# Performance work log

Hardware: AMD Instinct MI355X
Metric: run time of the kernel (lower is better)

## Reference

```python
import jax, jax.numpy as jnp
import numpy as np

N = 8192
K = 8192
BS = 128  # quantization block size (elements per codebook)
NE = 8    # codebook entries per block (3-bit indices)


def setup_inputs() -> dict:
    key = jax.random.key(0)
    k1, k2, k3 = jax.random.split(key, 3)
    num_blocks = N * K // BS  # 524288
    n_packed_bytes = num_blocks * BS * 3 // 8  # 25165824
    x = jax.random.normal(k1, (2048, K), dtype=jnp.float32)
    # random packed bytes (values 0..255) -> uniformly random 3-bit indices
    packed_indices = jax.random.randint(k2, (n_packed_bytes,), 0, 256, dtype=jnp.int32)
    codebook = jax.random.normal(k3, (num_blocks, NE), dtype=jnp.float32)
    return {"x": x, "packed_indices": packed_indices, "codebook": codebook}


def _dequantize(packed_indices, codebook):
    num_blocks = codebook.shape[0]
    packed = packed_indices.reshape(-1, 3).astype(jnp.int32)  # (n_groups, 3)
    bits24 = packed[:, 0] | (packed[:, 1] << 8) | (packed[:, 2] << 16)
    shifts = jnp.arange(8, dtype=jnp.int32) * 3
    idx = (bits24[:, None] >> shifts[None, :]) & 7          # (n_groups, 8)
    idx = idx.reshape(num_blocks, BS)                        # (num_blocks, BS)
    # per-block codebook gather: w[b, i] = codebook[b, idx[b, i]]
    w = jnp.take_along_axis(codebook, idx, axis=1)           # (num_blocks, BS)
    return w.reshape(N, K)


def reference(x, packed_indices, codebook):
    w = _dequantize(packed_indices, codebook)  # (N, K) fp32
    y = x @ w.T                                # (batch, N)
    return y
```

## Files before the change

### kernel.cpp

```cpp
#include <hip/hip_runtime.h>
#include <hip/hip_bf16.h>

#define Mdim 2048
#define Ndim 8192
#define Kdim 8192
#define NT (Kdim / 64)

typedef __bf16 bf16x8 __attribute__((ext_vector_type(8)));
typedef float f32x4 __attribute__((ext_vector_type(4)));
typedef unsigned short ushort8 __attribute__((ext_vector_type(8)));
typedef unsigned short ushort4v __attribute__((ext_vector_type(4)));

__device__ __forceinline__ unsigned short f2bf_rne(float f) {
    unsigned u = __float_as_uint(f);
    u += 0x7fffu + ((u >> 16) & 1u);
    return (unsigned short)(u >> 16);
}

__device__ __forceinline__ ushort8 decode8(unsigned bits, float4 c0, float4 c1) {
    ushort8 o;
#pragma unroll
    for (int i = 0; i < 8; ++i) {
        unsigned id = (bits >> (3 * i)) & 7u;
        float a0 = (id & 1) ? c0.y : c0.x;
        float a1 = (id & 1) ? c0.w : c0.z;
        float a2 = (id & 1) ? c1.y : c1.x;
        float a3 = (id & 1) ? c1.w : c1.z;
        float b0 = (id & 2) ? a1 : a0;
        float b1 = (id & 2) ? a3 : a2;
        float v  = (id & 4) ? b1 : b0;
        o[i] = f2bf_rne(v);
    }
    return o;
}

__global__ __launch_bounds__(256) void k_prep(const int* __restrict__ packed,
                                              const float* __restrict__ cb,
                                              const float* __restrict__ x,
                                              unsigned short* __restrict__ W,
                                              unsigned short* __restrict__ xb) {
    const int t = threadIdx.x;
    if (blockIdx.x < 16384) {
        const size_t th = (size_t)blockIdx.x * 256 + t;
        const size_t g0 = th * 2;
        const int2* pv = (const int2*)(packed + g0 * 3);
        int2 q0 = pv[0], q1 = pv[1], q2 = pv[2];
        unsigned bits0 = (unsigned)(q0.x & 255) | ((unsigned)(q0.y & 255) << 8) |
                         ((unsigned)(q1.x & 255) << 16);
        unsigned bits1 = (unsigned)(q1.y & 255) | ((unsigned)(q2.x & 255) << 8) |
                         ((unsigned)(q2.y & 255) << 16);
        const float4* cv0 = (const float4*)(cb + ((g0 >> 4) << 3));
        const float4* cv1 = (const float4*)(cb + (((g0 + 1) >> 4) << 3));
        float4 c00 = cv0[0], c01 = cv0[1];
        float4 c10 = cv1[0], c11 = cv1[1];
        ushort8 o0 = decode8(bits0, c00, c01);
        ushort8 o1 = decode8(bits1, c10, c11);
        unsigned short* wp = W + (g0 << 3);
        *(ushort8*)(wp)     = o0;
        *(ushort8*)(wp + 8) = o1;
    } else {
        const size_t u = (size_t)(blockIdx.x - 16384) * 256 + t;
        float4 a = ((const float4*)x)[u];
        ushort4v o;
        o[0] = f2bf_rne(a.x); o[1] = f2bf_rne(a.y);
        o[2] = f2bf_rne(a.z); o[3] = f2bf_rne(a.w);
        ((ushort4v*)xb)[u] = o;
    }
}

__device__ __forceinline__ void gld16(const unsigned short* g, unsigned short* l) {
    __builtin_amdgcn_global_load_lds(
        (const __attribute__((address_space(1))) unsigned int*)g,
        (__attribute__((address_space(3))) unsigned int*)l, 16, 0, 0);
}

#define BAR()    asm volatile("s_barrier" ::: "memory")
#define FENCE()  asm volatile("" ::: "memory")
#define WAIT_DS0() asm volatile("s_waitcnt lgkmcnt(0)" ::: "memory")

__global__ __launch_bounds__(512, 2) void k_gemm(const unsigned short* __restrict__ A,
                                                 const unsigned short* __restrict__ B,
                                                 float* __restrict__ C) {
    __shared__ unsigned short LA[4 * 8192];
    __shared__ unsigned short LB[4 * 8192];

    const int tid  = threadIdx.x;
    const int lane = tid & 63;
    const int wave = tid >> 6;
    const int qm = wave >> 2;
    const int qn = wave & 3;

    const int bid = blockIdx.x;
    const int bm = (bid & 7) * 256;
    const int bn = (bid >> 3) * 256;

    const int chunk0 = tid, chunk1 = tid + 512;
    const int srow0 = chunk0 >> 3, srow1 = chunk1 >> 3;
    const int scol0 = ((chunk0 & 7) ^ (srow0 & 7)) * 8;
    const int scol1 = ((chunk1 & 7) ^ (srow1 & 7)) * 8;
    const unsigned short* Ag0 = A + (size_t)(bm + srow0) * Kdim + scol0;
    const unsigned short* Ag1 = A + (size_t)(bm + srow1) * Kdim + scol1;
    const unsigned short* Bg0 = B + (size_t)(bn + srow0) * Kdim + scol0;
    const unsigned short* Bg1 = B + (size_t)(bn + srow1) * Kdim + scol1;

#define STAGE_A(T, H, BUF) do {                                                   \
    unsigned short* _d = LA + ((BUF) * 2 + (H)) * 8192;                           \
    gld16(Ag0 + (size_t)(H) * 128 * Kdim + (size_t)(T) * 64, _d + (size_t)tid * 8);        \
    gld16(Ag1 + (size_t)(H) * 128 * Kdim + (size_t)(T) * 64, _d + (size_t)(tid + 512) * 8);\
    FENCE();                                                                      \
} while (0)
#define STAGE_B(T, H, BUF) do {                                                   \
    unsigned short* _d = LB + ((BUF) * 2 + (H)) * 8192;                           \
    gld16(Bg0 + (size_t)(H) * 128 * Kdim + (size_t)(T) * 64, _d + (size_t)tid * 8);        \
    gld16(Bg1 + (size_t)(H) * 128 * Kdim + (size_t)(T) * 64, _d + (size_t)(tid + 512) * 8);\
    FENCE();                                                                      \
} while (0)

    const int r15 = lane & 15;
    const int q   = lane >> 4;
    const int rlo = r15 & 7;
    const int aro = qm * 64 + r15;
    const int bro = qn * 32 + r15;
    const int ch0 = ((0 + q) ^ rlo) * 8;
    const int ch1 = ((4 + q) ^ rlo) * 8;

    f32x4 acc[4][4][2];
    const f32x4 zero = {0.f, 0.f, 0.f, 0.f};
#pragma unroll
    for (int p = 0; p < 4; ++p)
#pragma unroll
        for (int i = 0; i < 4; ++i)
#pragma unroll
            for (int j = 0; j < 2; ++j) acc[p][i][j] = zero;

    bf16x8 af[4][2], bf[2][2];

#define LOAD_A(BUF, H) do {                                                       \
    const unsigned short* _s = LA + ((BUF) * 2 + (H)) * 8192;                     \
    _Pragma("unroll") for (int i = 0; i < 4; ++i) {                               \
        int _r = (aro + i * 16) * 64;                                             \
        af[i][0] = *(const bf16x8*)&_s[_r + ch0];                                 \
        af[i][1] = *(const bf16x8*)&_s[_r + ch1];                                 \
    }                                                                             \
} while (0)
#define LOAD_B(BUF, H) do {                                                       \
    const unsigned short* _s = LB + ((BUF) * 2 + (H)) * 8192;                     \
    _Pragma("unroll") for (int j = 0; j < 2; ++j) {                               \
        int _r = (bro + j * 16) * 64;                                             \
        bf[j][0] = *(const bf16x8*)&_s[_r + ch0];                                 \
        bf[j][1] = *(const bf16x8*)&_s[_r + ch1];                                 \
    }                                                                             \
} while (0)

#define MFMA_PHASE(P) do {                                                        \
    __builtin_amdgcn_s_setprio(1);                                                \
    _Pragma("unroll") for (int i = 0; i < 4; ++i)                                 \
    _Pragma("unroll") for (int j = 0; j < 2; ++j) {                               \
        acc[P][i][j] = __builtin_amdgcn_mfma_f32_16x16x32_bf16(                   \
            af[i][0], bf[j][0], acc[P][i][j], 0, 0, 0);                           \
        acc[P][i][j] = __builtin_amdgcn_mfma_f32_16x16x32_bf16(                   \
            af[i][1], bf[j][1], acc[P][i][j], 0, 0, 0);                           \
    }                                                                             \
    __builtin_amdgcn_s_setprio(0);                                                \
} while (0)

#define KSTEP(T, BUF) do {                                                        \
    LOAD_A(BUF, 0); LOAD_B(BUF, 0);                                               \
    if ((T) + 1 < NT) STAGE_B((T) + 1, 0, (BUF) ^ 1);                             \
    BAR(); WAIT_DS0();                                                            \
    MFMA_PHASE(0);                                                                \
    BAR();                                                                        \
    LOAD_B(BUF, 1);                                                               \
    if ((T) + 2 < NT) STAGE_A((T) + 2, 0, BUF);                                   \
    BAR(); WAIT_DS0();                                                            \
    MFMA_PHASE(1);                                                                \
    BAR();                                                                        \
    LOAD_A(BUF, 1);                                                               \
    if ((T) + 2 < NT) STAGE_B((T) + 2, 1, BUF);                                   \
    BAR(); WAIT_DS0();                                                            \
    MFMA_PHASE(2);                                                                \
    BAR();                                                                        \
    LOAD_B(BUF, 0);                                                               \
    if ((T) + 2 < NT) STAGE_A((T) + 2, 1, BUF);                                   \
    BAR(); WAIT_DS0();                                                            \
    MFMA_PHASE(3);                                                                \
    if ((T) + 2 < NT) { asm volatile("s_waitcnt vmcnt(6)" ::: "memory"); }        \
    else              { asm volatile("s_waitcnt vmcnt(0)" ::: "memory"); }        \
    BAR();                                                                        \
} while (0)

    STAGE_A(0, 0, 0); STAGE_B(0, 1, 0); STAGE_A(0, 1, 0); STAGE_B(0, 0, 0);
    STAGE_A(1, 0, 1); STAGE_B(1, 1, 1); STAGE_A(1, 1, 1);
    asm volatile("s_waitcnt vmcnt(6)" ::: "memory");
    BAR();

    for (int t2 = 0; t2 < NT; t2 += 2) {
        KSTEP(t2, 0);
        KSTEP(t2 + 1, 1);
    }

    constexpr int RHs[4] = {0, 0, 1, 1};
    constexpr int CHs[4] = {0, 1, 1, 0};
#pragma unroll
    for (int p = 0; p < 4; ++p) {
#pragma unroll
        for (int i = 0; i < 4; ++i) {
#pragma unroll
            for (int j = 0; j < 2; ++j) {
                int row = bm + RHs[p] * 128 + qm * 64 + i * 16 + q * 4;
                int col = bn + CHs[p] * 128 + qn * 32 + j * 16 + r15;
                float* outp = C + (size_t)row * Ndim + col;
#pragma unroll
                for (int r = 0; r < 4; ++r)
                    outp[(size_t)r * Ndim] = acc[p][i][j][r];
            }
        }
    }

#undef STAGE_A
#undef STAGE_B
#undef LOAD_A
#undef LOAD_B
#undef MFMA_PHASE
#undef KSTEP
}

extern "C" void kernel_launch(void* const* d_in, const int* in_sizes, int n_in,
                              void* d_out, int out_size, void* d_ws, size_t ws_size,
                              hipStream_t stream) {
    const float* x      = (const float*)d_in[0];
    const int*   packed = (const int*)d_in[1];
    const float* cb     = (const float*)d_in[2];
    float* out = (float*)d_out;

    unsigned short* Wb = (unsigned short*)d_ws;
    unsigned short* Xb = (unsigned short*)d_ws + (size_t)Ndim * Kdim;

    k_prep<<<32768, 256, 0, stream>>>(packed, cb, x, Wb, Xb);
    k_gemm<<<dim3(256), 512, 0, stream>>>(Xb, Wb, out);
}
```

Before: 473.0 us.

## Prefetch next-tile B fragments into registers and widen dequant prep per thread

The GEMM main loop is restructured so LDS fragment reads for the next k-tile (all B halves into a double-buffered register set, plus the next A half) are issued during the current MFMA phases. This removes the per-phase lgkmcnt(0) waits that stalled the matrix cores. Global stage issue order and vmcnt thresholds are reworked to match. The prep kernel now decodes four 3-bit groups per thread with int4 loads and one shared codebook fetch, halving the dequant grid. The register-prefetch design raises VGPR pressure, which under the (512,2) launch bound could spill. Relying on s_barrier without explicit LDS waits also risks ordering bugs.

```diff
diff --git a/kernel.cpp b/kernel.cpp
--- a/kernel.cpp
+++ b/kernel.cpp
@@ -40,26 +40,28 @@
                                               unsigned short* __restrict__ W,
                                               unsigned short* __restrict__ xb) {
     const int t = threadIdx.x;
-    if (blockIdx.x < 16384) {
+    if (blockIdx.x < 8192) {
         const size_t th = (size_t)blockIdx.x * 256 + t;
-        const size_t g0 = th * 2;
-        const int2* pv = (const int2*)(packed + g0 * 3);
-        int2 q0 = pv[0], q1 = pv[1], q2 = pv[2];
+        const size_t g0 = th * 4;
+        const int4* pv = (const int4*)(packed + g0 * 3);
+        int4 q0 = pv[0], q1 = pv[1], q2 = pv[2];
         unsigned bits0 = (unsigned)(q0.x & 255) | ((unsigned)(q0.y & 255) << 8) |
-                         ((unsigned)(q1.x & 255) << 16);
-        unsigned bits1 = (unsigned)(q1.y & 255) | ((unsigned)(q2.x & 255) << 8) |
-                         ((unsigned)(q2.y & 255) << 16);
-        const float4* cv0 = (const float4*)(cb + ((g0 >> 4) << 3));
-        const float4* cv1 = (const float4*)(cb + (((g0 + 1) >> 4) << 3));
-        float4 c00 = cv0[0], c01 = cv0[1];
-        float4 c10 = cv1[0], c11 = cv1[1];
-        ushort8 o0 = decode8(bits0, c00, c01);
-        ushort8 o1 = decode8(bits1, c10, c11);
+                         ((unsigned)(q0.z & 255) << 16);
+        unsigned bits1 = (unsigned)(q0.w & 255) | ((unsigned)(q1.x & 255) << 8) |
+                         ((unsigned)(q1.y & 255) << 16);
+        unsigned bits2 = (unsigned)(q1.z & 255) | ((unsigned)(q1.w & 255) << 8) |
+                         ((unsigned)(q2.x & 255) << 16);
+        unsigned bits3 = (unsigned)(q2.y & 255) | ((unsigned)(q2.z & 255) << 8) |
+                         ((unsigned)(q2.w & 255) << 16);
+        const float4* cv = (const float4*)(cb + ((g0 >> 4) << 3));
+        float4 c0 = cv[0], c1 = cv[1];
         unsigned short* wp = W + (g0 << 3);
-        *(ushort8*)(wp)     = o0;
-        *(ushort8*)(wp + 8) = o1;
+        *(ushort8*)(wp)      = decode8(bits0, c0, c1);
+        *(ushort8*)(wp + 8)  = decode8(bits1, c0, c1);
+        *(ushort8*)(wp + 16) = decode8(bits2, c0, c1);
+        *(ushort8*)(wp + 24) = decode8(bits3, c0, c1);
     } else {
-        const size_t u = (size_t)(blockIdx.x - 16384) * 256 + t;
+        const size_t u = (size_t)(blockIdx.x - 8192) * 256 + t;
         float4 a = ((const float4*)x)[u];
         ushort4v o;
         o[0] = f2bf_rne(a.x); o[1] = f2bf_rne(a.y);
@@ -76,7 +78,8 @@
 
 #define BAR()    asm volatile("s_barrier" ::: "memory")
 #define FENCE()  asm volatile("" ::: "memory")
-#define WAIT_DS0() asm volatile("s_waitcnt lgkmcnt(0)" ::: "memory")
+#define SBAR0()  __builtin_amdgcn_sched_barrier(0)
+#define VMCNT(n) asm volatile("s_waitcnt vmcnt(" #n ")" ::: "memory")
 
 __global__ __launch_bounds__(512, 2) void k_gemm(const unsigned short* __restrict__ A,
                                                  const unsigned short* __restrict__ B,
@@ -133,70 +136,80 @@
 #pragma unroll
             for (int j = 0; j < 2; ++j) acc[p][i][j] = zero;
 
-    bf16x8 af[4][2], bf[2][2];
-
-#define LOAD_A(BUF, H) do {                                                       \
+    bf16x8 aF[4][2];
+    bf16x8 bX[2][2][2];
+    bf16x8 bY[2][2][2];
+
+#define LOAD_AF(BUF, H) do {                                                      \
     const unsigned short* _s = LA + ((BUF) * 2 + (H)) * 8192;                     \
     _Pragma("unroll") for (int i = 0; i < 4; ++i) {                               \
         int _r = (aro + i * 16) * 64;                                             \
-        af[i][0] = *(const bf16x8*)&_s[_r + ch0];                                 \
-        af[i][1] = *(const bf16x8*)&_s[_r + ch1];                                 \
-    }                                                                             \
-} while (0)
-#define LOAD_B(BUF, H) do {                                                       \
-    const unsigned short* _s = LB + ((BUF) * 2 + (H)) * 8192;                     \
-    _Pragma("unroll") for (int j = 0; j < 2; ++j) {                               \
-        int _r = (bro + j * 16) * 64;                                             \
-        bf[j][0] = *(const bf16x8*)&_s[_r + ch0];                                 \
-        bf[j][1] = *(const bf16x8*)&_s[_r + ch1];                                 \
-    }                                                                             \
-} while (0)
-
-#define MFMA_PHASE(P) do {                                                        \
+        aF[i][0] = *(const bf16x8*)&_s[_r + ch0];                                 \
+        aF[i][1] = *(const bf16x8*)&_s[_r + ch1];                                 \
+    }                                                                             \
+} while (0)
+#define LOAD_BALL(BUF, BSET) do {                                                 \
+    _Pragma("unroll") for (int _h = 0; _h < 2; ++_h) {                            \
+        const unsigned short* _s = LB + ((BUF) * 2 + _h) * 8192;                  \
+        _Pragma("unroll") for (int j = 0; j < 2; ++j) {                           \
+            int _r = (bro + j * 16) * 64;                                         \
+            BSET[_h][j][0] = *(const bf16x8*)&_s[_r + ch0];                       \
+            BSET[_h][j][1] = *(const bf16x8*)&_s[_r + ch1];                       \
+        }                                                                         \
+    }                                                                             \
+} while (0)
+
+#define MFMA_PH(P, BSET, H) do {                                                  \
     __builtin_amdgcn_s_setprio(1);                                                \
     _Pragma("unroll") for (int i = 0; i < 4; ++i)                                 \
     _Pragma("unroll") for (int j = 0; j < 2; ++j) {                               \
         acc[P][i][j] = __builtin_amdgcn_mfma_f32_16x16x32_bf16(                   \
-            af[i][0], bf[j][0], acc[P][i][j], 0, 0, 0);                           \
+            aF[i][0], BSET[(H)][j][0], acc[P][i][j], 0, 0, 0);                    \
         acc[P][i][j] = __builtin_amdgcn_mfma_f32_16x16x32_bf16(                   \
-            af[i][1], bf[j][1], acc[P][i][j], 0, 0, 0);                           \
+            aF[i][1], BSET[(H)][j][1], acc[P][i][j], 0, 0, 0);                    \
     }                                                                             \
     __builtin_amdgcn_s_setprio(0);                                                \
 } while (0)
 
-#define KSTEP(T, BUF) do {                                                        \
-    LOAD_A(BUF, 0); LOAD_B(BUF, 0);                                               \
-    if ((T) + 1 < NT) STAGE_B((T) + 1, 0, (BUF) ^ 1);                             \
-    BAR(); WAIT_DS0();                                                            \
-    MFMA_PHASE(0);                                                                \
-    BAR();                                                                        \
-    LOAD_B(BUF, 1);                                                               \
+#define KSTEP(T, BUF, BCUR, BNXT) do {                                            \
+                                                                          \
+    if ((T) + 1 < NT) { VMCNT(6); STAGE_A((T) + 1, 1, (BUF) ^ 1); }               \
+    else              { VMCNT(0); }                                               \
+    MFMA_PH(0, BCUR, 0);                                                          \
+    BAR();                                                                        \
+                                                                          \
+    if ((T) + 1 < NT) { VMCNT(4); }                                               \
+    if ((T) + 2 < NT) STAGE_B((T) + 2, 0, BUF);                                   \
+    MFMA_PH(1, BCUR, 1);                                                          \
+    SBAR0();                                                                      \
+    LOAD_AF(BUF, 1);                      \
+    BAR();                                                                        \
+                                                                          \
+    if ((T) + 1 < NT) {                                                           \
+        if ((T) + 2 < NT) { VMCNT(4); } else { VMCNT(2); }                        \
+        LOAD_BALL((BUF) ^ 1, BNXT);                                               \
+    }                                                                             \
+    if ((T) + 2 < NT) STAGE_B((T) + 2, 1, BUF);                                   \
+    MFMA_PH(2, BCUR, 1);                                                          \
+    BAR();                                                                        \
+                                                                          \
     if ((T) + 2 < NT) STAGE_A((T) + 2, 0, BUF);                                   \
-    BAR(); WAIT_DS0();                                                            \
-    MFMA_PHASE(1);                                                                \
-    BAR();                                                                        \
-    LOAD_A(BUF, 1);                                                               \
-    if ((T) + 2 < NT) STAGE_B((T) + 2, 1, BUF);                                   \
-    BAR(); WAIT_DS0();                                                            \
-    MFMA_PHASE(2);                                                                \
-    BAR();                                                                        \
-    LOAD_B(BUF, 0);                                                               \
-    if ((T) + 2 < NT) STAGE_A((T) + 2, 1, BUF);                                   \
-    BAR(); WAIT_DS0();                                                            \
-    MFMA_PHASE(3);                                                                \
-    if ((T) + 2 < NT) { asm volatile("s_waitcnt vmcnt(6)" ::: "memory"); }        \
-    else              { asm volatile("s_waitcnt vmcnt(0)" ::: "memory"); }        \
-    BAR();                                                                        \
-} while (0)
-
-    STAGE_A(0, 0, 0); STAGE_B(0, 1, 0); STAGE_A(0, 1, 0); STAGE_B(0, 0, 0);
-    STAGE_A(1, 0, 1); STAGE_B(1, 1, 1); STAGE_A(1, 1, 1);
-    asm volatile("s_waitcnt vmcnt(6)" ::: "memory");
+    MFMA_PH(3, BCUR, 0);                                                          \
+    SBAR0();                                                                      \
+    if ((T) + 1 < NT) LOAD_AF((BUF) ^ 1, 0);                \
+    BAR();                                                                        \
+} while (0)
+
+    STAGE_B(0, 0, 0); STAGE_B(0, 1, 0); STAGE_A(0, 0, 0); STAGE_A(0, 1, 0);
+    STAGE_B(1, 0, 1); STAGE_B(1, 1, 1); STAGE_A(1, 0, 1);
+    asm volatile("s_waitcnt vmcnt(8)" ::: "memory");
     BAR();
+    LOAD_BALL(0, bX);
+    LOAD_AF(0, 0);
 
     for (int t2 = 0; t2 < NT; t2 += 2) {
-        KSTEP(t2, 0);
-        KSTEP(t2 + 1, 1);
+        KSTEP(t2, 0, bX, bY);
+        KSTEP(t2 + 1, 1, bY, bX);
     }
 
     constexpr int RHs[4] = {0, 0, 1, 1};
@@ -219,9 +232,9 @@
 
 #undef STAGE_A
 #undef STAGE_B
-#undef LOAD_A
-#undef LOAD_B
-#undef MFMA_PHASE
+#undef LOAD_AF
+#undef LOAD_BALL
+#undef MFMA_PH
 #undef KSTEP
 }
 
@@ -236,6 +249,6 @@
     unsigned short* Wb = (unsigned short*)d_ws;
     unsigned short* Xb = (unsigned short*)d_ws + (size_t)Ndim * Kdim;
 
-    k_prep<<<32768, 256, 0, stream>>>(packed, cb, x, Wb, Xb);
+    k_prep<<<24576, 256, 0, stream>>>(packed, cb, x, Wb, Xb);
     k_gemm<<<dim3(256), 512, 0, stream>>>(Xb, Wb, out);
 }
```

Result: no change. 471.3 us (-0.4%).
